# Performance work log

Hardware: AMD Instinct MI355X
Metric: run time of the kernel (lower is better)

Reference implementation:

```python
import jax, jax.numpy as jnp
import numpy as np

N_EMBD = 1024
N_HEAD = 16
HEAD_SIZE = 64

def setup_inputs() -> dict:
    key = jax.random.key(0)
    ks = jax.random.split(key, 6)
    B, T = 4, 2048
    x = jax.random.normal(ks[0], (B, T, N_EMBD), dtype=jnp.float32)
    s = 1.0 / np.sqrt(N_EMBD)
    Wq = jax.random.normal(ks[1], (N_HEAD, N_EMBD, HEAD_SIZE), dtype=jnp.float32) * s
    Wk = jax.random.normal(ks[2], (N_HEAD, N_EMBD, HEAD_SIZE), dtype=jnp.float32) * s
    Wv = jax.random.normal(ks[3], (N_HEAD, N_EMBD, HEAD_SIZE), dtype=jnp.float32) * s
    Wp = jax.random.normal(ks[4], (N_EMBD, N_EMBD), dtype=jnp.float32) * s
    bp = jax.random.normal(ks[5], (N_EMBD,), dtype=jnp.float32) * 0.01
    return {"x": x, "Wq": Wq, "Wk": Wk, "Wv": Wv, "Wp": Wp, "bp": bp}

def reference(x, Wq, Wk, Wv, Wp, bp):
    B, T, C = x.shape
    # per-head projections, all heads at once: [B,H,T,hs]
    q = jnp.einsum('btc,hcd->bhtd', x, Wq)
    k = jnp.einsum('btc,hcd->bhtd', x, Wk)
    v = jnp.einsum('btc,hcd->bhtd', x, Wv)
    # NOTE: original scales by C**-0.5 with C = n_embd (not head_size)
    scale = C ** (-0.5)
    wei = jnp.einsum('bhtd,bhsd->bhts', q, k) * scale  # [B,H,T,T]
    causal = jnp.tril(jnp.ones((T, T), dtype=bool))
    wei = jnp.where(causal, wei, -jnp.inf)
    wei = jax.nn.softmax(wei, axis=-1)
    out = jnp.einsum('bhts,bhsd->bhtd', wei, v)  # [B,H,T,hs]
    out = out.transpose(0, 2, 1, 3).reshape(B, T, -1)  # concat heads -> [B,T,C]
    return out @ Wp + bp
```

## Files before the change

### kernel.cpp

```cpp
#include <hip/hip_runtime.h>
#include <stdint.h>
#include <math.h>

typedef short s16x8 __attribute__((ext_vector_type(8)));
typedef float f32x4 __attribute__((ext_vector_type(4)));
typedef float f32x16 __attribute__((ext_vector_type(16)));

__device__ __forceinline__ unsigned short f2bf(float f) {
    union { float f; uint32_t u; } x; x.f = f;
    uint32_t r = x.u + 0x7FFFu + ((x.u >> 16) & 1u);
    return (unsigned short)(r >> 16);
}

__device__ __forceinline__ uint32_t cvtpk_bf16(float lo, float hi) {
    uint32_t r;
    asm("v_cvt_pk_bf16_f32 %0, %1, %2" : "=v"(r) : "v"(lo), "v"(hi));
    return r;
}

#define GLD_LDS16(gp, lp) __builtin_amdgcn_global_load_lds( \
    (const __attribute__((address_space(1))) uint32_t*)(gp), \
    (__attribute__((address_space(3))) uint32_t*)(lp), 16, 0, 0)

#define MFMA16x16x32(a, b, c) __builtin_amdgcn_mfma_f32_16x16x32_bf16((a), (b), (c), 0, 0, 0)
#define MFMA32x32x16(a, b, c) __builtin_amdgcn_mfma_f32_32x32x16_bf16((a), (b), (c), 0, 0, 0)

__device__ __forceinline__ void plswap(uint32_t a, uint32_t b, int lh, uint32_t& x, uint32_t& y) {
#if __has_builtin(__builtin_amdgcn_permlane32_swap)
    auto r = __builtin_amdgcn_permlane32_swap(a, b, false, false);
    x = (uint32_t)r[0]; y = (uint32_t)r[1];
#else
    uint32_t as = (uint32_t)__shfl_xor((int)a, 32, 64);
    uint32_t bs = (uint32_t)__shfl_xor((int)b, 32, 64);
    x = lh ? bs : a;
    y = lh ? b : as;
#endif
}

__global__ void cvt_x_kernel(const float* __restrict__ x, unsigned short* __restrict__ xb, int n) {
    int i = (blockIdx.x * blockDim.x + threadIdx.x) * 4;
    if (i >= n) return;
    float4 v = *(const float4*)(x + i);
    unsigned short o0 = f2bf(v.x), o1 = f2bf(v.y), o2 = f2bf(v.z), o3 = f2bf(v.w);
    uint64_t packed = (uint64_t)o0 | ((uint64_t)o1 << 16) | ((uint64_t)o2 << 32) | ((uint64_t)o3 << 48);
    *(uint64_t*)(xb + i) = packed;
}

__global__ void cvt_w_kernel(const float* __restrict__ Wq, const float* __restrict__ Wk,
                             const float* __restrict__ Wv, const float* __restrict__ Wp,
                             unsigned short* __restrict__ WtQKV, unsigned short* __restrict__ WtP) {
    int id = (blockIdx.x * blockDim.x + threadIdx.x) * 4;
    int which = id >> 20, rem = id & 1048575;
    const float* src = (which == 0) ? Wq : (which == 1) ? Wk : (which == 2) ? Wv : Wp;
    float4 v = *(const float4*)(src + rem);
    unsigned short* dst;
    if (which < 3) {
        int h = rem >> 16, c = (rem >> 6) & 1023, d = rem & 63;
        dst = WtQKV + (size_t)(which * 1024 + h * 64 + d) * 1024 + c;
    } else {
        int c = rem >> 10, n = rem & 1023;
        dst = WtP + (size_t)n * 1024 + c;
    }
    dst[0] = f2bf(v.x); dst[1024] = f2bf(v.y); dst[2048] = f2bf(v.z); dst[3072] = f2bf(v.w);
}

template<int MODE>
__global__ __launch_bounds__(256) void gemm_bt_kernel(
    const unsigned short* __restrict__ A, const unsigned short* __restrict__ Bt,
    void* __restrict__ Cv, unsigned short* __restrict__ vT,
    const float* __restrict__ bias, int M, int N, int K)
{
    constexpr int BK = 64;
    __shared__ __align__(16) unsigned short As[128 * BK];
    __shared__ __align__(16) unsigned short Bs[128 * BK];
    const int t = threadIdx.x, w = t >> 6, l = t & 63, lr = l & 15, lg = l >> 4;
    const int wm = (w >> 1) << 6, wn = (w & 1) << 6;
    const int bm = blockIdx.x << 7, bn = blockIdx.y << 7;
    const unsigned short* Ab = A + (size_t)bm * K;
    const unsigned short* Bb = Bt + (size_t)bn * K;
    f32x4 acc[4][4] = {};
    for (int k0 = 0; k0 < K; k0 += BK) {
        __syncthreads();
        #pragma unroll
        for (int i = 0; i < 4; ++i) {
            int c = i * 256 + t;
            GLD_LDS16(Ab + (size_t)(c >> 3) * K + k0 + ((c & 7) << 3), As + c * 8);
        }
        #pragma unroll
        for (int i = 0; i < 4; ++i) {
            int c = i * 256 + t;
            GLD_LDS16(Bb + (size_t)(c >> 3) * K + k0 + ((c & 7) << 3), Bs + c * 8);
        }
        __syncthreads();
        #pragma unroll
        for (int ks = 0; ks < 2; ++ks) {
            s16x8 af[4], bfr[4];
            #pragma unroll
            for (int mi = 0; mi < 4; ++mi)
                af[mi] = *(const s16x8*)&As[(wm + mi * 16 + lr) * BK + ks * 32 + lg * 8];
            #pragma unroll
            for (int ni = 0; ni < 4; ++ni)
                bfr[ni] = *(const s16x8*)&Bs[(wn + ni * 16 + lr) * BK + ks * 32 + lg * 8];
            #pragma unroll
            for (int mi = 0; mi < 4; ++mi)
                #pragma unroll
                for (int ni = 0; ni < 4; ++ni)
                    acc[mi][ni] = MFMA16x16x32(af[mi], bfr[ni], acc[mi][ni]);
        }
    }
    if (MODE == 1) {
        float* C = (float*)Cv;
        #pragma unroll
        for (int mi = 0; mi < 4; ++mi)
            #pragma unroll
            for (int ni = 0; ni < 4; ++ni) {
                int col = bn + wn + ni * 16 + lr;
                float bv = bias ? bias[col] : 0.0f;
                #pragma unroll
                for (int r = 0; r < 4; ++r) {
                    int row = bm + wm + mi * 16 + lg * 4 + r;
                    C[(size_t)row * N + col] = acc[mi][ni][r] + bv;
                }
            }
    } else {
        unsigned short* Cq = (unsigned short*)Cv;
        const bool isV = (bn >= 2048);
        const float sc = (bn < 1024) ? (0.03125f * 1.44269504088896341f) : 1.0f;
        #pragma unroll
        for (int mi = 0; mi < 4; ++mi)
            #pragma unroll
            for (int ni = 0; ni < 4; ++ni) {
                int col = bn + wn + ni * 16 + lr;
                int row0 = bm + wm + mi * 16 + lg * 4;
                if (!isV) {
                    #pragma unroll
                    for (int r = 0; r < 4; ++r)
                        Cq[(size_t)(row0 + r) * 2048 + col] = f2bf(acc[mi][ni][r] * sc);
                } else {
                    int h = (col >> 6) & 15, d = col & 63;
                    size_t vb = ((size_t)((row0 >> 11) * 16 + h) * 64 + d) * 2048 + (row0 & 2047);
                    uint32_t u0 = (uint32_t)f2bf(acc[mi][ni][0]) | ((uint32_t)f2bf(acc[mi][ni][1]) << 16);
                    uint32_t u1 = (uint32_t)f2bf(acc[mi][ni][2]) | ((uint32_t)f2bf(acc[mi][ni][3]) << 16);
                    *(uint32_t*)&vT[vb]     = u0;
                    *(uint32_t*)&vT[vb + 2] = u1;
                }
            }
    }
}

__device__ __forceinline__ void proc32(
    const unsigned short* __restrict__ Ksb, const unsigned short* __restrict__ Vtb,
    const s16x8* qf, f32x16* o, float& m_r, float& l_r,
    int qms, bool domask, int lq, int lh)
{
    const int ub = lq >> 1;
    const int vb8 = (lq & 1) << 3;
    f32x16 S[2] = {};
    __builtin_amdgcn_s_setprio(1);
    #pragma unroll
    for (int sblk = 0; sblk < 2; ++sblk)
        #pragma unroll
        for (int kd = 0; kd < 4; ++kd) {
            s16x8 kf = *(const s16x8*)((const char*)Ksb + (sblk * 16 + ub) * 256
                                       + ((((2 * kd + lh) + vb8) ^ ub) << 4));
            S[sblk] = MFMA32x32x16(kf, qf[kd], S[sblk]);
        }
    __builtin_amdgcn_s_setprio(0);
    if (domask) {
        #pragma unroll
        for (int sblk = 0; sblk < 2; ++sblk)
            #pragma unroll
            for (int r = 0; r < 16; ++r) {
                int s_loc = sblk * 32 + (r & 3) + 8 * (r >> 2) + 4 * lh;
                S[sblk][r] = (s_loc <= qms) ? S[sblk][r] : -1e30f;
            }
    }
    float zm = S[0][0];
    #pragma unroll
    for (int r = 1; r < 15; r += 2) zm = fmaxf(fmaxf(zm, S[0][r]), S[0][r + 1]);
    zm = fmaxf(zm, S[0][15]);
    #pragma unroll
    for (int r = 0; r < 16; r += 2) zm = fmaxf(fmaxf(zm, S[1][r]), S[1][r + 1]);
    zm = fmaxf(zm, __shfl_xor(zm, 32, 64));
    const bool defer = (__all(zm <= m_r + 8.0f) != 0);
    if (!defer) {
        float mn = fmaxf(m_r, zm);
        float alpha = exp2f(m_r - mn);
        m_r = mn;
        l_r *= alpha;
        o[0] *= alpha;
        o[1] *= alpha;
    }
    float rs = 0.0f;
    uint32_t pk[2][8];
    #pragma unroll
    for (int sblk = 0; sblk < 2; ++sblk) {
        #pragma unroll
        for (int r = 0; r < 16; ++r) {
            float pv = exp2f(S[sblk][r] - m_r);
            S[sblk][r] = pv;
            rs += pv;
        }
        #pragma unroll
        for (int hh = 0; hh < 8; ++hh)
            pk[sblk][hh] = cvtpk_bf16(S[sblk][2 * hh], S[sblk][2 * hh + 1]);
    }
    rs += __shfl_xor(rs, 32, 64);
    l_r += rs;
    s16x8 pf[4];
    #pragma unroll
    for (int ks2 = 0; ks2 < 4; ++ks2) {
        int sb = ks2 >> 1, Bh = 4 * (ks2 & 1);
        uint32_t w0, w1, w2, w3;
        plswap(pk[sb][Bh + 0], pk[sb][Bh + 2], lh, w0, w2);
        plswap(pk[sb][Bh + 1], pk[sb][Bh + 3], lh, w1, w3);
        union { uint32_t u[4]; s16x8 v; } pu;
        pu.u[0] = w0; pu.u[1] = w1; pu.u[2] = w2; pu.u[3] = w3;
        pf[ks2] = pu.v;
    }
    __builtin_amdgcn_s_setprio(1);
    #pragma unroll
    for (int dblk = 0; dblk < 2; ++dblk)
        #pragma unroll
        for (int ks2 = 0; ks2 < 4; ++ks2) {
            s16x8 vf = *(const s16x8*)((const char*)Vtb + (dblk * 16 + ub) * 256
                                       + ((((2 * ks2 + lh) + vb8) ^ ub) << 4));
            o[dblk] = MFMA32x32x16(vf, pf[ks2], o[dblk]);
        }
    __builtin_amdgcn_s_setprio(0);
}

__global__ __launch_bounds__(512, 4) void attn_kernel(
    const unsigned short* __restrict__ qkv2, const unsigned short* __restrict__ vT,
    unsigned short* __restrict__ attnO, int T)
{
    __shared__ __align__(16) unsigned short Ks[2][64 * 64];
    __shared__ __align__(16) unsigned short Vt[2][64 * 64];

    const int blk = blockIdx.x;
    const int p = blk & 7, h = (blk >> 3) & 15, b = blk >> 7;
    const int q0A = p * 128, q0B = (15 - p) * 128;
    const int nkv = 32 - 2 * p;

    const int t = threadIdx.x, w = t >> 6, l = t & 63, lq = l & 31, lh = l >> 5;
    const int c0 = ((w >> 2) ? q0B : q0A) + 32 * (w & 3);
    const int lastT = (c0 + 31) >> 6;

    const unsigned short* qbase = qkv2 + (size_t)b * T * 2048;
    const unsigned short* kbase = qbase + 1024 + h * 64;
    const unsigned short* vtb   = vT + (size_t)(b * 16 + h) * 64 * 2048;

    s16x8 qf[4];
    #pragma unroll
    for (int kd = 0; kd < 4; ++kd)
        qf[kd] = *(const s16x8*)(qbase + (size_t)(c0 + lq) * 2048 + h * 64 + kd * 16 + lh * 8);

    f32x16 o[2] = {};
    float m_r = -1e30f, l_r = 0.0f;

    const int su = t >> 4, sx = (t & 15) ^ (su & 15);
    const int srow = 2 * su + (sx >> 3), schunk = (sx & 7) << 3;
    auto STAGE = [&](int buf, int s0) {
        GLD_LDS16(kbase + (size_t)(s0 + srow) * 2048 + schunk, &Ks[buf][t * 8]);
        GLD_LDS16(vtb + (size_t)srow * 2048 + s0 + schunk, &Vt[buf][t * 8]);
    };

    STAGE(0, 0);
    __syncthreads();

    for (int kt = 0; kt < nkv; ++kt) {
        const int cur = kt & 1, nxt = cur ^ 1;
        if (kt + 1 < nkv) STAGE(nxt, (kt + 1) * 64);
        if (kt <= lastT)
            proc32(Ks[cur], Vt[cur], qf, o, m_r, l_r, c0 + lq - kt * 64, kt == lastT, lq, lh);
        __syncthreads();
    }

    {
        float inv = 1.0f / l_r;
        #pragma unroll
        for (int dblk = 0; dblk < 2; ++dblk)
            #pragma unroll
            for (int r = 0; r < 16; r += 2) {
                int d = dblk * 32 + (r & 3) + 8 * (r >> 2) + 4 * lh;
                uint32_t ua = cvtpk_bf16(o[dblk][r] * inv, o[dblk][r + 1] * inv);
                *(uint32_t*)&attnO[(size_t)(b * T + c0 + lq) * 1024 + h * 64 + d] = ua;
            }
    }
}

extern "C" void kernel_launch(void* const* d_in, const int* in_sizes, int n_in,
                              void* d_out, int out_size, void* d_ws, size_t ws_size,
                              hipStream_t stream) {
    const float* x  = (const float*)d_in[0];
    const float* Wq = (const float*)d_in[1];
    const float* Wk = (const float*)d_in[2];
    const float* Wv = (const float*)d_in[3];
    const float* Wp = (const float*)d_in[4];
    const float* bp = (const float*)d_in[5];
    float* out = (float*)d_out;

    const int T = 2048, C = 1024;
    const int BT = in_sizes[0] / C;
    const int B  = BT / T;

    char* ws = (char*)d_ws;
    unsigned short* xb    = (unsigned short*)(ws);
    unsigned short* WtQKV = (unsigned short*)(ws + 16777216);
    unsigned short* WtP   = (unsigned short*)(ws + 23068672);
    unsigned short* qkv2  = (unsigned short*)(ws + 25165824);
    unsigned short* vT    = (unsigned short*)(ws + 58720256);
    unsigned short* attn  = (unsigned short*)(ws + 75497472);
    (void)ws_size; (void)n_in; (void)out_size;

    cvt_x_kernel<<<(BT * C / 4 + 255) / 256, 256, 0, stream>>>(x, xb, BT * C);
    cvt_w_kernel<<<4096, 256, 0, stream>>>(Wq, Wk, Wv, Wp, WtQKV, WtP);

    gemm_bt_kernel<0><<<dim3(BT / 128, 3072 / 128), 256, 0, stream>>>(
        xb, WtQKV, qkv2, vT, nullptr, BT, 3072, C);

    attn_kernel<<<B * 16 * 8, 512, 0, stream>>>(qkv2, vT, attn, T);

    gemm_bt_kernel<1><<<dim3(BT / 128, 1024 / 128), 256, 0, stream>>>(
        attn, WtP, out, nullptr, bp, BT, 1024, C);
}
```

Measured before the change: 213.6 us.

## Rewrite QKV GEMM with triple-buffered LDS pipeline, 128x256 tiles and swizzles

Replaces the templated QKV projection GEMM with a dedicated kernel. It uses 512 threads, 128x256 output tiles and BK=32, with a three-stage LDS ring so global-to-LDS loads for step j+2 overlap the MFMA work for step j. LDS layout is XOR-swizzled to avoid bank conflicts, and the block index is remapped for L2 locality. The output projection GEMM keeps the old design, split out as its own kernel. The cost is more complex manual waitcnt and barrier scheduling, with a risk of subtle race bugs.

Measured after the change: 198.4 us. 7.1% less time.

```diff
diff --git a/kernel.cpp b/kernel.cpp
--- a/kernel.cpp
+++ b/kernel.cpp
@@ -64,11 +64,125 @@
     dst[0] = f2bf(v.x); dst[1024] = f2bf(v.y); dst[2048] = f2bf(v.z); dst[3072] = f2bf(v.w);
 }
 
-template<int MODE>
-__global__ __launch_bounds__(256) void gemm_bt_kernel(
+__global__ __launch_bounds__(512, 4) void gemm_qkv_kernel(
     const unsigned short* __restrict__ A, const unsigned short* __restrict__ Bt,
-    void* __restrict__ Cv, unsigned short* __restrict__ vT,
-    const float* __restrict__ bias, int M, int N, int K)
+    unsigned short* __restrict__ qkv2, unsigned short* __restrict__ vT)
+{
+    constexpr int K = 1024, NT = 32;
+    __shared__ __align__(16) unsigned short LA[3][128 * 32];
+    __shared__ __align__(16) unsigned short LB[3][256 * 32];
+
+    const int t = threadIdx.x, w = t >> 6, l = t & 63, lr = l & 15, lg = l >> 4;
+    const int wm2 = w >> 2, wn4 = w & 3;
+
+    int bid = blockIdx.x;
+    int swz = (bid & 7) * 96 + (bid >> 3);
+    const int bm = (swz & 63) << 7, bn = (swz >> 6) << 8;
+
+    const unsigned short* Ab = A + (size_t)bm * K;
+    const unsigned short* Bb = Bt + (size_t)bn * K;
+
+    int sArow, sAce, sBrow[2], sBce[2];
+    {
+        int u = t >> 4, x = (t & 15) ^ (u & 15);
+        sArow = 4 * u + (x >> 2); sAce = (x & 3) << 3;
+        #pragma unroll
+        for (int i2 = 0; i2 < 2; ++i2) {
+            int i = t + i2 * 512;
+            int ub = i >> 4, xb2 = (i & 15) ^ (ub & 15);
+            sBrow[i2] = 4 * ub + (xb2 >> 2); sBce[i2] = (xb2 & 3) << 3;
+        }
+    }
+
+    int aoff[4], boff[4];
+    #pragma unroll
+    for (int m = 0; m < 4; ++m) {
+        int u = 16 * wm2 + 4 * m + (lr >> 2);
+        aoff[m] = u * 256 + (((lg + 4 * (lr & 3)) ^ (u & 15)) << 4);
+    }
+    #pragma unroll
+    for (int n = 0; n < 4; ++n) {
+        int u = 16 * wn4 + 4 * n + (lr >> 2);
+        boff[n] = u * 256 + (((lg + 4 * (lr & 3)) ^ (u & 15)) << 4);
+    }
+
+    f32x4 acc[4][4] = {};
+
+    GLD_LDS16(Ab + (size_t)sArow * K + 0 + sAce, &LA[0][t * 8]);
+    #pragma unroll
+    for (int i2 = 0; i2 < 2; ++i2)
+        GLD_LDS16(Bb + (size_t)sBrow[i2] * K + 0 + sBce[i2], &LB[0][(t + i2 * 512) * 8]);
+    GLD_LDS16(Ab + (size_t)sArow * K + 32 + sAce, &LA[1][t * 8]);
+    #pragma unroll
+    for (int i2 = 0; i2 < 2; ++i2)
+        GLD_LDS16(Bb + (size_t)sBrow[i2] * K + 32 + sBce[i2], &LB[1][(t + i2 * 512) * 8]);
+    asm volatile("s_waitcnt vmcnt(3)" ::: "memory");
+    __builtin_amdgcn_sched_barrier(0);
+    __builtin_amdgcn_s_barrier();
+
+    int cur = 0;
+    for (int j = 0; j < NT; ++j) {
+        const int dst = (cur >= 1) ? cur - 1 : cur + 2;
+        const bool st = (j + 2 < NT);
+        const int k2 = (j + 2) << 5;
+        s16x8 af[4], bfr[4];
+        #pragma unroll
+        for (int m = 0; m < 4; ++m)
+            af[m] = *(const s16x8*)((const char*)LA[cur] + aoff[m]);
+        #pragma unroll
+        for (int n = 0; n < 4; ++n)
+            bfr[n] = *(const s16x8*)((const char*)LB[cur] + boff[n]);
+        if (st) {
+            GLD_LDS16(Ab + (size_t)sArow * K + k2 + sAce, &LA[dst][t * 8]);
+            #pragma unroll
+            for (int i2 = 0; i2 < 2; ++i2)
+                GLD_LDS16(Bb + (size_t)sBrow[i2] * K + k2 + sBce[i2], &LB[dst][(t + i2 * 512) * 8]);
+        }
+        __builtin_amdgcn_s_barrier();
+        asm volatile("s_waitcnt lgkmcnt(0)" ::: "memory");
+        __builtin_amdgcn_sched_barrier(0);
+        __builtin_amdgcn_s_setprio(1);
+        #pragma unroll
+        for (int m = 0; m < 4; ++m)
+            #pragma unroll
+            for (int n = 0; n < 4; ++n)
+                acc[m][n] = MFMA16x16x32(af[m], bfr[n], acc[m][n]);
+        __builtin_amdgcn_s_setprio(0);
+        if (j + 1 < NT) {
+            if (st) { asm volatile("s_waitcnt vmcnt(3)" ::: "memory"); }
+            else    { asm volatile("s_waitcnt vmcnt(0)" ::: "memory"); }
+            __builtin_amdgcn_sched_barrier(0);
+        }
+        __builtin_amdgcn_s_barrier();
+        cur = (cur == 2) ? 0 : cur + 1;
+    }
+
+    const bool isV = (bn >= 2048);
+    const float sc = (bn < 1024) ? (0.03125f * 1.44269504088896341f) : 1.0f;
+    #pragma unroll
+    for (int mi = 0; mi < 4; ++mi)
+        #pragma unroll
+        for (int ni = 0; ni < 4; ++ni) {
+            int col = bn + wn4 * 64 + ni * 16 + lr;
+            int row0 = bm + wm2 * 64 + mi * 16 + lg * 4;
+            if (!isV) {
+                #pragma unroll
+                for (int r = 0; r < 4; ++r)
+                    qkv2[(size_t)(row0 + r) * 2048 + col] = f2bf(acc[mi][ni][r] * sc);
+            } else {
+                int h = (col >> 6) & 15, d = col & 63;
+                size_t vb = ((size_t)((row0 >> 11) * 16 + h) * 64 + d) * 2048 + (row0 & 2047);
+                uint32_t u0 = (uint32_t)f2bf(acc[mi][ni][0]) | ((uint32_t)f2bf(acc[mi][ni][1]) << 16);
+                uint32_t u1 = (uint32_t)f2bf(acc[mi][ni][2]) | ((uint32_t)f2bf(acc[mi][ni][3]) << 16);
+                *(uint32_t*)&vT[vb]     = u0;
+                *(uint32_t*)&vT[vb + 2] = u1;
+            }
+        }
+}
+
+__global__ __launch_bounds__(256) void gemm_proj_kernel(
+    const unsigned short* __restrict__ A, const unsigned short* __restrict__ Bt,
+    float* __restrict__ C, const float* __restrict__ bias, int M, int N, int K)
 {
     constexpr int BK = 64;
     __shared__ __align__(16) unsigned short As[128 * BK];
@@ -108,44 +222,18 @@
                     acc[mi][ni] = MFMA16x16x32(af[mi], bfr[ni], acc[mi][ni]);
         }
     }
-    if (MODE == 1) {
-        float* C = (float*)Cv;
-        #pragma unroll
-        for (int mi = 0; mi < 4; ++mi)
-            #pragma unroll
-            for (int ni = 0; ni < 4; ++ni) {
-                int col = bn + wn + ni * 16 + lr;
-                float bv = bias ? bias[col] : 0.0f;
-                #pragma unroll
-                for (int r = 0; r < 4; ++r) {
-                    int row = bm + wm + mi * 16 + lg * 4 + r;
-                    C[(size_t)row * N + col] = acc[mi][ni][r] + bv;
-                }
+    #pragma unroll
+    for (int mi = 0; mi < 4; ++mi)
+        #pragma unroll
+        for (int ni = 0; ni < 4; ++ni) {
+            int col = bn + wn + ni * 16 + lr;
+            float bv = bias[col];
+            #pragma unroll
+            for (int r = 0; r < 4; ++r) {
+                int row = bm + wm + mi * 16 + lg * 4 + r;
+                C[(size_t)row * N + col] = acc[mi][ni][r] + bv;
             }
-    } else {
-        unsigned short* Cq = (unsigned short*)Cv;
-        const bool isV = (bn >= 2048);
-        const float sc = (bn < 1024) ? (0.03125f * 1.44269504088896341f) : 1.0f;
-        #pragma unroll
-        for (int mi = 0; mi < 4; ++mi)
-            #pragma unroll
-            for (int ni = 0; ni < 4; ++ni) {
-                int col = bn + wn + ni * 16 + lr;
-                int row0 = bm + wm + mi * 16 + lg * 4;
-                if (!isV) {
-                    #pragma unroll
-                    for (int r = 0; r < 4; ++r)
-                        Cq[(size_t)(row0 + r) * 2048 + col] = f2bf(acc[mi][ni][r] * sc);
-                } else {
-                    int h = (col >> 6) & 15, d = col & 63;
-                    size_t vb = ((size_t)((row0 >> 11) * 16 + h) * 64 + d) * 2048 + (row0 & 2047);
-                    uint32_t u0 = (uint32_t)f2bf(acc[mi][ni][0]) | ((uint32_t)f2bf(acc[mi][ni][1]) << 16);
-                    uint32_t u1 = (uint32_t)f2bf(acc[mi][ni][2]) | ((uint32_t)f2bf(acc[mi][ni][3]) << 16);
-                    *(uint32_t*)&vT[vb]     = u0;
-                    *(uint32_t*)&vT[vb + 2] = u1;
-                }
-            }
-    }
+        }
 }
 
 __device__ __forceinline__ void proc32(
@@ -316,11 +404,10 @@
     cvt_x_kernel<<<(BT * C / 4 + 255) / 256, 256, 0, stream>>>(x, xb, BT * C);
     cvt_w_kernel<<<4096, 256, 0, stream>>>(Wq, Wk, Wv, Wp, WtQKV, WtP);
 
-    gemm_bt_kernel<0><<<dim3(BT / 128, 3072 / 128), 256, 0, stream>>>(
-        xb, WtQKV, qkv2, vT, nullptr, BT, 3072, C);
+    gemm_qkv_kernel<<<768, 512, 0, stream>>>(xb, WtQKV, qkv2, vT);
 
     attn_kernel<<<B * 16 * 8, 512, 0, stream>>>(qkv2, vT, attn, T);
 
-    gemm_bt_kernel<1><<<dim3(BT / 128, 1024 / 128), 256, 0, stream>>>(
-        attn, WtP, out, nullptr, bp, BT, 1024, C);
-}
+    gemm_proj_kernel<<<dim3(BT / 128, 1024 / 128), 256, 0, stream>>>(
+        attn, WtP, out, bp, BT, 1024, C);
+}
```
